# Kernel tuning notes

Hardware: AMD Instinct MI355X
Metric: run time of the kernel (lower is better)

## Reference

```python
import jax, jax.numpy as jnp
import numpy as np

N_NODES = 100000
N_EDGES = 1600000
D_IN = 128
D_HID = 128
N_CLS = 2


def gcn_conv(x, edge_index, W, b):
    """PyG GCNConv: add self-loops, symmetric normalization, linear, scatter-add, bias."""
    n = x.shape[0]
    loop = jnp.arange(n, dtype=edge_index.dtype)
    src = jnp.concatenate([edge_index[0], loop])  # [E+N]
    dst = jnp.concatenate([edge_index[1], loop])
    # degree computed on destination (col) after adding self-loops
    deg = jax.ops.segment_sum(jnp.ones_like(dst, dtype=x.dtype), dst, num_segments=n)
    dinv = jnp.where(deg > 0, jax.lax.rsqrt(deg), 0.0)
    norm = dinv[src] * dinv[dst]  # [E+N]
    h = x @ W  # [N, out]
    msg = h[src] * norm[:, None]  # [E+N, out]
    out = jax.ops.segment_sum(msg, dst, num_segments=n)
    return out + b


def setup_inputs() -> dict:
    key = jax.random.key(0)
    k1, k2, k3, k4 = jax.random.split(key, 4)
    x = jax.random.normal(k1, (N_NODES, D_IN), dtype=jnp.float32)
    edge_index = jax.random.randint(k2, (2, N_EDGES), 0, N_NODES, dtype=jnp.int64)
    W1 = jax.random.normal(k3, (D_IN, D_HID), dtype=jnp.float32) * (1.0 / np.sqrt(D_IN))
    b1 = jnp.zeros((D_HID,), dtype=jnp.float32)
    W2 = jax.random.normal(k4, (D_HID, N_CLS), dtype=jnp.float32) * (1.0 / np.sqrt(D_HID))
    b2 = jnp.zeros((N_CLS,), dtype=jnp.float32)
    return {"x": x, "edge_index": edge_index, "W1": W1, "b1": b1, "W2": W2, "b2": b2}


def reference(x, edge_index, W1, b1, W2, b2):
    h = gcn_conv(x, edge_index, W1, b1)
    h = jax.nn.relu(h)
    # training=False -> dropout skipped
    out = gcn_conv(h, edge_index, W2, b2)
    return out
```

## Files before the change

### kernel.cpp

```cpp
#include <hip/hip_runtime.h>
#include <hip/hip_fp16.h>
#include <cstdint>
#include <cstddef>

#define NN 100000
#define NE 1600000
#define D 128
#define NBK 782
#define NBLK_P 200
#define EPB 8000

typedef _Float16 half8 __attribute__((ext_vector_type(8)));
typedef _Float16 half4v __attribute__((ext_vector_type(4)));
typedef float f32x4 __attribute__((ext_vector_type(4)));


__launch_bounds__(256)
__global__ void p1_count_k(const int* __restrict__ ei, unsigned* __restrict__ offs) {
    __shared__ unsigned hist[NBK];
    int tid = threadIdx.x, b = blockIdx.x;
    for (int k = tid; k < NBK; k += 256) hist[k] = 0u;
    __syncthreads();
    int e0 = b * EPB;
    for (int i = tid; i < EPB; i += 256) {
        int d = ei[NE + e0 + i];
        atomicAdd(&hist[d >> 7], 1u);
    }
    __syncthreads();
    for (int k = tid; k < NBK; k += 256) offs[(size_t)b * NBK + k] = hist[k];
}

__launch_bounds__(256)
__global__ void p2a_k(unsigned* __restrict__ offs, unsigned* __restrict__ base) {
    __shared__ unsigned sh[256];
    int t = threadIdx.x, k = blockIdx.x;
    unsigned v = (t < NBLK_P) ? offs[(size_t)t * NBK + k] : 0u;
    sh[t] = v;
    __syncthreads();
    for (int off = 1; off < 256; off <<= 1) {
        unsigned u = (t >= off) ? sh[t - off] : 0u;
        __syncthreads();
        sh[t] += u;
        __syncthreads();
    }
    if (t < NBLK_P) offs[(size_t)t * NBK + k] = sh[t] - v;
    if (t == 255) base[k] = sh[255];
}

__global__ void p2b_k(unsigned* __restrict__ base) {
    __shared__ unsigned sh[1024];
    int t = threadIdx.x;
    unsigned v = (t < NBK) ? base[t] : 0u;
    sh[t] = v;
    __syncthreads();
    for (int off = 1; off < 1024; off <<= 1) {
        unsigned u = (t >= off) ? sh[t - off] : 0u;
        __syncthreads();
        sh[t] += u;
        __syncthreads();
    }
    if (t < NBK) base[t] = sh[t] - v;
    if (t == NBK) base[NBK] = sh[NBK - 1];
}

__launch_bounds__(256)
__global__ void p3_scatter_k(const int* __restrict__ ei, const unsigned* __restrict__ offs,
                             const unsigned* __restrict__ base, unsigned* __restrict__ part) {
    __shared__ unsigned lcnt[NBK];
    int tid = threadIdx.x, b = blockIdx.x;
    for (int k = tid; k < NBK; k += 256) lcnt[k] = base[k] + offs[(size_t)b * NBK + k];
    __syncthreads();
    int e0 = b * EPB;
    for (int i = tid; i < EPB; i += 256) {
        int s = ei[e0 + i];
        int d = ei[NE + e0 + i];
        unsigned pos = atomicAdd(&lcnt[d >> 7], 1u);
        part[pos] = (unsigned)s | ((unsigned)(d & 127) << 20);
    }
}

__launch_bounds__(256)
__global__ void p4_csr_k(const unsigned* __restrict__ part, const unsigned* __restrict__ base,
                         unsigned* __restrict__ rp, float* __restrict__ dinv,
                         unsigned* __restrict__ col) {
    __shared__ unsigned c[128], p[128], run[128];
    int tid = threadIdx.x, k = blockIdx.x;
    int n0 = k << 7;
    int nodes = (NN - n0 < 128) ? (NN - n0) : 128;
    unsigned e0 = base[k], e1 = base[k + 1];

    if (tid < 128) c[tid] = 0u;
    __syncthreads();
    for (unsigned e = e0 + tid; e < e1; e += 256)
        atomicAdd(&c[(part[e] >> 20) & 127], 1u);
    __syncthreads();

    unsigned myc = (tid < 128) ? c[tid] : 0u;
    if (tid < 128) p[tid] = myc;
    __syncthreads();
    for (int off = 1; off < 128; off <<= 1) {
        unsigned u = 0;
        if (tid < 128 && tid >= off) u = p[tid - off];
        __syncthreads();
        if (tid < 128) p[tid] += u;
        __syncthreads();
    }
    if (tid < 128) {
        unsigned excl = p[tid] - myc;
        run[tid] = excl;
        if (tid < nodes) {
            rp[n0 + tid] = e0 + excl;
            dinv[n0 + tid] = rsqrtf((float)(myc + 1u));
        }
    }
    if (k == 0 && tid == 0) rp[NN] = NE;
    __syncthreads();

    for (unsigned e = e0 + tid; e < e1; e += 256) {
        unsigned v = part[e];
        unsigned dlo = (v >> 20) & 127;
        unsigned pos = e0 + atomicAdd(&run[dlo], 1u);
        col[pos] = v & 0xFFFFFu;
    }
}

__global__ void wt_k(const float* __restrict__ W, _Float16* __restrict__ Wt) {
    int idx = blockIdx.x * 256 + threadIdx.x;
    int n = idx >> 7, k = idx & 127;
    Wt[idx] = (_Float16)W[k * 128 + n];
}

__launch_bounds__(256)
__global__ void gemm1_k(const float* __restrict__ x, const _Float16* __restrict__ Wt,
                        const float* __restrict__ dinv, _Float16* __restrict__ h) {
    __shared__ _Float16 wt[128 * 136];
    __shared__ _Float16 xs[64 * 136];
    int tid = threadIdx.x;
    int rb = blockIdx.x * 64;
    int w = tid >> 6, lane = tid & 63;
    int m = lane & 15, q4 = lane >> 4;

#pragma unroll
    for (int q = 0; q < 8; q++) {
        int idx = q * 256 + tid;
        int n  = idx >> 4;
        int k8 = (idx & 15) * 8;
        *(half8*)(&wt[n * 136 + k8]) = *(const half8*)(Wt + n * 128 + k8);
    }
#pragma unroll
    for (int q = 0; q < 8; q++) {
        int idx = q * 256 + tid;
        int row = idx >> 5;
        int c4 = (idx & 31) * 4;
        int gr = rb + row;
        float4 v = (gr < NN) ? *(const float4*)(x + (size_t)gr * 128 + c4)
                             : make_float4(0, 0, 0, 0);
        half4v hv = { (_Float16)v.x, (_Float16)v.y, (_Float16)v.z, (_Float16)v.w };
        *(half4v*)(&xs[row * 136 + c4]) = hv;
    }
    __syncthreads();

    f32x4 acc[8];
#pragma unroll
    for (int nt = 0; nt < 8; nt++) acc[nt] = (f32x4){0.f, 0.f, 0.f, 0.f};

    const _Float16* arow = &xs[(w * 16 + m) * 136 + q4 * 8];
#pragma unroll
    for (int kc = 0; kc < 4; kc++) {
        half8 af = *(const half8*)(arow + kc * 32);
#pragma unroll
        for (int nt = 0; nt < 8; nt++) {
            half8 bf = *(const half8*)(&wt[(nt * 16 + m) * 136 + q4 * 8 + kc * 32]);
            acc[nt] = __builtin_amdgcn_mfma_f32_16x16x32_f16(af, bf, acc[nt], 0, 0, 0);
        }
    }

    float dv[4];
#pragma unroll
    for (int r = 0; r < 4; r++) {
        int ri = rb + w * 16 + q4 * 4 + r;
        dv[r] = (ri < NN) ? dinv[ri] : 0.f;
    }
    __syncthreads();
#pragma unroll
    for (int nt = 0; nt < 8; nt++) {
#pragma unroll
        for (int r = 0; r < 4; r++) {
            xs[(w * 16 + q4 * 4 + r) * 136 + nt * 16 + m] = (_Float16)(acc[nt][r] * dv[r]);
        }
    }
    __syncthreads();
#pragma unroll
    for (int q = 0; q < 4; q++) {
        int idx = q * 256 + tid;
        int row = idx >> 4;
        int c8 = (idx & 15) * 8;
        int gr = rb + row;
        if (gr < NN)
            *(half8*)(h + (size_t)gr * 128 + c8) = *(const half8*)(&xs[row * 136 + c8]);
    }
}

__launch_bounds__(256)
__global__ void agg1_k(const _Float16* __restrict__ h, const unsigned* __restrict__ rp,
                       const unsigned* __restrict__ col, const float* __restrict__ dinv,
                       const float* __restrict__ b1, const float* __restrict__ W2,
                       float* __restrict__ z) {
    int i = (blockIdx.x * 256 + threadIdx.x) >> 6;
    int lane = threadIdx.x & 63;
    if (i >= NN) return;

    const __half2* hb = (const __half2*)h;
    float di = dinv[i];
    float2 hv = __half22float2(hb[(size_t)i * 64 + lane]);
    float ax = hv.x, ay = hv.y;

    unsigned p0 = __builtin_amdgcn_readfirstlane(rp[i]);
    unsigned p1 = __builtin_amdgcn_readfirstlane(rp[i + 1]);
    unsigned e = p0;
    for (; e + 8 <= p1; e += 8) {
        unsigned s0 = __builtin_amdgcn_readfirstlane(col[e]);
        unsigned s1 = __builtin_amdgcn_readfirstlane(col[e + 1]);
        unsigned s2 = __builtin_amdgcn_readfirstlane(col[e + 2]);
        unsigned s3 = __builtin_amdgcn_readfirstlane(col[e + 3]);
        unsigned s4 = __builtin_amdgcn_readfirstlane(col[e + 4]);
        unsigned s5 = __builtin_amdgcn_readfirstlane(col[e + 5]);
        unsigned s6 = __builtin_amdgcn_readfirstlane(col[e + 6]);
        unsigned s7 = __builtin_amdgcn_readfirstlane(col[e + 7]);
        float2 v0 = __half22float2(hb[(size_t)(s0 * 64u + lane)]);
        float2 v1 = __half22float2(hb[(size_t)(s1 * 64u + lane)]);
        float2 v2 = __half22float2(hb[(size_t)(s2 * 64u + lane)]);
        float2 v3 = __half22float2(hb[(size_t)(s3 * 64u + lane)]);
        float2 v4 = __half22float2(hb[(size_t)(s4 * 64u + lane)]);
        float2 v5 = __half22float2(hb[(size_t)(s5 * 64u + lane)]);
        float2 v6 = __half22float2(hb[(size_t)(s6 * 64u + lane)]);
        float2 v7 = __half22float2(hb[(size_t)(s7 * 64u + lane)]);
        ax += v0.x + v1.x + v2.x + v3.x + v4.x + v5.x + v6.x + v7.x;
        ay += v0.y + v1.y + v2.y + v3.y + v4.y + v5.y + v6.y + v7.y;
    }
    for (; e < p1; ++e) {
        unsigned s = __builtin_amdgcn_readfirstlane(col[e]);
        float2 v = __half22float2(hb[(size_t)(s * 64u + lane)]);
        ax += v.x;
        ay += v.y;
    }
    ax *= di;
    ay *= di;

    float2 bv = ((const float2*)b1)[lane];
    float h0 = fmaxf(ax + bv.x, 0.f);
    float h1 = fmaxf(ay + bv.y, 0.f);

    float4 w = ((const float4*)W2)[lane];
    float pz0 = fmaf(h0, w.x, h1 * w.z);
    float pz1 = fmaf(h0, w.y, h1 * w.w);
#pragma unroll
    for (int off = 32; off > 0; off >>= 1) {
        pz0 += __shfl_down(pz0, off);
        pz1 += __shfl_down(pz1, off);
    }
    if (lane == 0) {
        float2* zp = (float2*)(z + (size_t)i * 2);
        *zp = make_float2(pz0 * di, pz1 * di);
    }
}

__launch_bounds__(256)
__global__ void agg2_k(const float* __restrict__ z, const unsigned* __restrict__ rp,
                       const unsigned* __restrict__ col, const float* __restrict__ dinv,
                       const float* __restrict__ b2, float* __restrict__ out) {
    int i = (blockIdx.x * 256 + threadIdx.x) >> 6;
    int lane = threadIdx.x & 63;
    if (i >= NN) return;

    float di = dinv[i];
    unsigned p0 = __builtin_amdgcn_readfirstlane(rp[i]);
    unsigned p1 = __builtin_amdgcn_readfirstlane(rp[i + 1]);
    float a0 = 0.f, a1 = 0.f;
    for (unsigned e = p0 + lane; e < p1; e += 64) {
        unsigned s = col[e];
        float2 v = ((const float2*)z)[s];
        a0 += v.x;
        a1 += v.y;
    }
#pragma unroll
    for (int off = 32; off > 0; off >>= 1) {
        a0 += __shfl_down(a0, off);
        a1 += __shfl_down(a1, off);
    }
    if (lane == 0) {
        float2 zi = ((const float2*)z)[i];
        out[(size_t)i * 2]     = (a0 + zi.x) * di + b2[0];
        out[(size_t)i * 2 + 1] = (a1 + zi.y) * di + b2[1];
    }
}

extern "C" void kernel_launch(void* const* d_in, const int* in_sizes, int n_in,
                              void* d_out, int out_size, void* d_ws, size_t ws_size,
                              hipStream_t stream) {
    const float* x  = (const float*)d_in[0];
    const int*   ei = (const int*)d_in[1];
    const float* W1 = (const float*)d_in[2];
    const float* b1 = (const float*)d_in[3];
    const float* W2 = (const float*)d_in[4];
    const float* b2 = (const float*)d_in[5];
    float* out = (float*)d_out;

    char* ws = (char*)d_ws;
    unsigned* part = (unsigned*)(ws);
    unsigned* offs = (unsigned*)(ws + 6400000);
    unsigned* base = (unsigned*)(ws + 7100000);
    _Float16* h    = (_Float16*)(ws);
    float*    z    = (float*)(ws + 25600000);
    float*    dinv = (float*)(ws + 26400000);
    unsigned* rp   = (unsigned*)(ws + 26800000);
    unsigned* col  = (unsigned*)(ws + 27200016);
    _Float16* Wt   = (_Float16*)(ws + 33600016);

    wt_k<<<64, 256, 0, stream>>>(W1, Wt);
    p1_count_k<<<NBLK_P, 256, 0, stream>>>(ei, offs);
    p2a_k<<<NBK, 256, 0, stream>>>(offs, base);
    p2b_k<<<1, 1024, 0, stream>>>(base);
    p3_scatter_k<<<NBLK_P, 256, 0, stream>>>(ei, offs, base, part);
    p4_csr_k<<<NBK, 256, 0, stream>>>(part, base, rp, dinv, col);

    gemm1_k<<<(NN + 63) / 64, 256, 0, stream>>>(x, Wt, dinv, h);
    agg1_k<<<(NN + 3) / 4, 256, 0, stream>>>(h, rp, col, dinv, b1, W2, z);
    agg2_k<<<(NN + 3) / 4, 256, 0, stream>>>(z, rp, col, dinv, b2, out);
}
```

Measured before the change: 242.7 us.

## Use more partition blocks, read W from global in GEMM, unroll gather by 16

Three separate changes. The CSR build now uses 512 partition blocks of 3125 edges each, with the column scan widened to 512 threads, so the count and scatter phases get more parallelism. The GEMM drops its shared-memory copy of W and reads B fragments straight from global/L2, which frees LDS and removes one staging pass. The layer-1 aggregation unrolls the neighbour gather to 16 with a tree reduction and adds a 4-wide tail, putting more loads in flight per wave.

```diff
diff --git a/kernel.cpp b/kernel.cpp
--- a/kernel.cpp
+++ b/kernel.cpp
@@ -7,8 +7,8 @@
 #define NE 1600000
 #define D 128
 #define NBK 782
-#define NBLK_P 200
-#define EPB 8000
+#define NBLK_P 512
+#define EPB 3125
 
 typedef _Float16 half8 __attribute__((ext_vector_type(8)));
 typedef _Float16 half4v __attribute__((ext_vector_type(4)));
@@ -30,21 +30,21 @@
     for (int k = tid; k < NBK; k += 256) offs[(size_t)b * NBK + k] = hist[k];
 }
 
-__launch_bounds__(256)
+__launch_bounds__(512)
 __global__ void p2a_k(unsigned* __restrict__ offs, unsigned* __restrict__ base) {
-    __shared__ unsigned sh[256];
+    __shared__ unsigned sh[512];
     int t = threadIdx.x, k = blockIdx.x;
-    unsigned v = (t < NBLK_P) ? offs[(size_t)t * NBK + k] : 0u;
+    unsigned v = offs[(size_t)t * NBK + k];
     sh[t] = v;
     __syncthreads();
-    for (int off = 1; off < 256; off <<= 1) {
+    for (int off = 1; off < 512; off <<= 1) {
         unsigned u = (t >= off) ? sh[t - off] : 0u;
         __syncthreads();
         sh[t] += u;
         __syncthreads();
     }
-    if (t < NBLK_P) offs[(size_t)t * NBK + k] = sh[t] - v;
-    if (t == 255) base[k] = sh[255];
+    offs[(size_t)t * NBK + k] = sh[t] - v;
+    if (t == 511) base[k] = sh[511];
 }
 
 __global__ void p2b_k(unsigned* __restrict__ base) {
@@ -133,20 +133,12 @@
 __launch_bounds__(256)
 __global__ void gemm1_k(const float* __restrict__ x, const _Float16* __restrict__ Wt,
                         const float* __restrict__ dinv, _Float16* __restrict__ h) {
-    __shared__ _Float16 wt[128 * 136];
     __shared__ _Float16 xs[64 * 136];
     int tid = threadIdx.x;
     int rb = blockIdx.x * 64;
     int w = tid >> 6, lane = tid & 63;
     int m = lane & 15, q4 = lane >> 4;
 
-#pragma unroll
-    for (int q = 0; q < 8; q++) {
-        int idx = q * 256 + tid;
-        int n  = idx >> 4;
-        int k8 = (idx & 15) * 8;
-        *(half8*)(&wt[n * 136 + k8]) = *(const half8*)(Wt + n * 128 + k8);
-    }
 #pragma unroll
     for (int q = 0; q < 8; q++) {
         int idx = q * 256 + tid;
@@ -165,12 +157,13 @@
     for (int nt = 0; nt < 8; nt++) acc[nt] = (f32x4){0.f, 0.f, 0.f, 0.f};
 
     const _Float16* arow = &xs[(w * 16 + m) * 136 + q4 * 8];
+    const _Float16* brow = Wt + m * 128 + q4 * 8;
 #pragma unroll
     for (int kc = 0; kc < 4; kc++) {
         half8 af = *(const half8*)(arow + kc * 32);
 #pragma unroll
         for (int nt = 0; nt < 8; nt++) {
-            half8 bf = *(const half8*)(&wt[(nt * 16 + m) * 136 + q4 * 8 + kc * 32]);
+            half8 bf = *(const half8*)(brow + nt * 16 * 128 + kc * 32);
             acc[nt] = __builtin_amdgcn_mfma_f32_16x16x32_f16(af, bf, acc[nt], 0, 0, 0);
         }
     }
@@ -201,6 +194,10 @@
     }
 }
 
+#define GATHER(sv, vv) \
+    { unsigned s_ = __builtin_amdgcn_readfirstlane(col[sv]); \
+      vv = __half22float2(hb[(size_t)(s_ * 64u + lane)]); }
+
 __launch_bounds__(256)
 __global__ void agg1_k(const _Float16* __restrict__ h, const unsigned* __restrict__ rp,
                        const unsigned* __restrict__ col, const float* __restrict__ dinv,
@@ -218,29 +215,26 @@
     unsigned p0 = __builtin_amdgcn_readfirstlane(rp[i]);
     unsigned p1 = __builtin_amdgcn_readfirstlane(rp[i + 1]);
     unsigned e = p0;
-    for (; e + 8 <= p1; e += 8) {
-        unsigned s0 = __builtin_amdgcn_readfirstlane(col[e]);
-        unsigned s1 = __builtin_amdgcn_readfirstlane(col[e + 1]);
-        unsigned s2 = __builtin_amdgcn_readfirstlane(col[e + 2]);
-        unsigned s3 = __builtin_amdgcn_readfirstlane(col[e + 3]);
-        unsigned s4 = __builtin_amdgcn_readfirstlane(col[e + 4]);
-        unsigned s5 = __builtin_amdgcn_readfirstlane(col[e + 5]);
-        unsigned s6 = __builtin_amdgcn_readfirstlane(col[e + 6]);
-        unsigned s7 = __builtin_amdgcn_readfirstlane(col[e + 7]);
-        float2 v0 = __half22float2(hb[(size_t)(s0 * 64u + lane)]);
-        float2 v1 = __half22float2(hb[(size_t)(s1 * 64u + lane)]);
-        float2 v2 = __half22float2(hb[(size_t)(s2 * 64u + lane)]);
-        float2 v3 = __half22float2(hb[(size_t)(s3 * 64u + lane)]);
-        float2 v4 = __half22float2(hb[(size_t)(s4 * 64u + lane)]);
-        float2 v5 = __half22float2(hb[(size_t)(s5 * 64u + lane)]);
-        float2 v6 = __half22float2(hb[(size_t)(s6 * 64u + lane)]);
-        float2 v7 = __half22float2(hb[(size_t)(s7 * 64u + lane)]);
-        ax += v0.x + v1.x + v2.x + v3.x + v4.x + v5.x + v6.x + v7.x;
-        ay += v0.y + v1.y + v2.y + v3.y + v4.y + v5.y + v6.y + v7.y;
+    for (; e + 16 <= p1; e += 16) {
+        float2 v0, v1, v2, v3, v4, v5, v6, v7, v8, v9, va, vb, vc, vd, ve, vf;
+        GATHER(e, v0)      GATHER(e + 1, v1)  GATHER(e + 2, v2)  GATHER(e + 3, v3)
+        GATHER(e + 4, v4)  GATHER(e + 5, v5)  GATHER(e + 6, v6)  GATHER(e + 7, v7)
+        GATHER(e + 8, v8)  GATHER(e + 9, v9)  GATHER(e + 10, va) GATHER(e + 11, vb)
+        GATHER(e + 12, vc) GATHER(e + 13, vd) GATHER(e + 14, ve) GATHER(e + 15, vf)
+        ax += ((v0.x + v1.x) + (v2.x + v3.x)) + ((v4.x + v5.x) + (v6.x + v7.x))
+            + ((v8.x + v9.x) + (va.x + vb.x)) + ((vc.x + vd.x) + (ve.x + vf.x));
+        ay += ((v0.y + v1.y) + (v2.y + v3.y)) + ((v4.y + v5.y) + (v6.y + v7.y))
+            + ((v8.y + v9.y) + (va.y + vb.y)) + ((vc.y + vd.y) + (ve.y + vf.y));
+    }
+    for (; e + 4 <= p1; e += 4) {
+        float2 v0, v1, v2, v3;
+        GATHER(e, v0) GATHER(e + 1, v1) GATHER(e + 2, v2) GATHER(e + 3, v3)
+        ax += (v0.x + v1.x) + (v2.x + v3.x);
+        ay += (v0.y + v1.y) + (v2.y + v3.y);
     }
     for (; e < p1; ++e) {
-        unsigned s = __builtin_amdgcn_readfirstlane(col[e]);
-        float2 v = __half22float2(hb[(size_t)(s * 64u + lane)]);
+        float2 v;
+        GATHER(e, v)
         ax += v.x;
         ay += v.y;
     }
@@ -309,7 +303,7 @@
     char* ws = (char*)d_ws;
     unsigned* part = (unsigned*)(ws);
     unsigned* offs = (unsigned*)(ws + 6400000);
-    unsigned* base = (unsigned*)(ws + 7100000);
+    unsigned* base = (unsigned*)(ws + 8100000);
     _Float16* h    = (_Float16*)(ws);
     float*    z    = (float*)(ws + 25600000);
     float*    dinv = (float*)(ws + 26400000);
@@ -319,7 +313,7 @@
 
     wt_k<<<64, 256, 0, stream>>>(W1, Wt);
     p1_count_k<<<NBLK_P, 256, 0, stream>>>(ei, offs);
-    p2a_k<<<NBK, 256, 0, stream>>>(offs, base);
+    p2a_k<<<NBK, 512, 0, stream>>>(offs, base);
     p2b_k<<<1, 1024, 0, stream>>>(base);
     p3_scatter_k<<<NBLK_P, 256, 0, stream>>>(ei, offs, base, part);
     p4_csr_k<<<NBK, 256, 0, stream>>>(part, base, rp, dinv, col);
```

Result: slower. 262.7 us (+8.2%).
